# Kernel tuning notes

Hardware: AMD Instinct MI355X
Metric: run time of the kernel (lower is better)

Reference implementation:

```python
import jax, jax.numpy as jnp
import numpy as np

NUM_M = 2_000_000
NUM_T = 512
N = 16
NUM_GEN = N * (N - 1) // 2  # 120
NUM_STEPS = 64
TAU = 1.0


def _make_bases():
    # skew-symmetric so(n) basis, matching the torch buffer construction order
    bases = np.zeros((NUM_GEN, N, N), np.float32)
    k = 0
    for i in range(N):
        for j in range(i + 1, N):
            bases[k, i, j] = -1.0
            bases[k, j, i] = 1.0
            k += 1
    return jnp.asarray(bases)


def setup_inputs() -> dict:
    key = jax.random.key(0)
    ks = jax.random.split(key, 8)
    W = jax.random.normal(ks[0], (NUM_M, N), jnp.float32)
    emb_weight = W / jnp.linalg.norm(W, axis=-1, keepdims=True)  # normalized at init
    transition_coeffs = jax.random.normal(ks[1], (NUM_T, NUM_GEN), jnp.float32) * 0.1

    def lin(k, fi, fo):  # torch nn.Linear default init
        bound = 1.0 / np.sqrt(fi)
        kw, kb = jax.random.split(k)
        w = jax.random.uniform(kw, (fi, fo), jnp.float32, -bound, bound)
        b = jax.random.uniform(kb, (fo,), jnp.float32, -bound, bound)
        return w, b

    w1, b1 = lin(ks[2], 2 * N, 256)
    w2, b2 = lin(ks[3], 256, 128)
    w3, b3 = lin(ks[4], 128, NUM_T)

    v_src = jax.random.uniform(ks[5], (1, NUM_M), jnp.float32)
    v_target = jax.random.uniform(ks[6], (1, NUM_M), jnp.float32)
    # pre-sampled Gumbel(0,1) noise for gumbel_softmax, one draw per step
    u = jax.random.uniform(ks[7], (NUM_STEPS, 1, NUM_T), jnp.float32, 1e-6, 1.0 - 1e-6)
    gumbel = -jnp.log(-jnp.log(u))

    return {
        'v_src': v_src, 'v_target': v_target,
        'emb_weight': emb_weight, 'transition_coeffs': transition_coeffs,
        'bases': _make_bases(),
        'w1': w1, 'b1': b1, 'w2': w2, 'b2': b2, 'w3': w3, 'b3': b3,
        'gumbel': gumbel, 'num_steps': NUM_STEPS,
    }


def reference(v_src, v_target, emb_weight, transition_coeffs, bases,
              w1, b1, w2, b2, w3, b3, gumbel, num_steps):
    # training=True path of PetriNetAlignmentPredictor.forward, tau=1.0
    embs = emb_weight / jnp.linalg.norm(emb_weight, axis=-1, keepdims=True)
    v_cur = v_src @ embs      # [1, n]  (memory-bound matvec over num_m)
    v_tgt = v_target @ embs   # [1, n]
    gens = jnp.einsum('tg,gnm->tnm', transition_coeffs, bases)  # [num_t, n, n]
    expm_b = jax.vmap(jax.scipy.linalg.expm)

    def step(v, g):
        h = jax.nn.relu(jnp.concatenate([v, v_tgt], axis=-1) @ w1 + b1)
        h = jax.nn.relu(h @ w2 + b2)
        logits = h @ w3 + b3                       # [1, num_t]
        # gumbel_softmax(hard=True) with straight-through estimator
        y = jax.nn.softmax((logits + g) / TAU, axis=-1)
        hard = jax.nn.one_hot(jnp.argmax(y, axis=-1), logits.shape[-1], dtype=y.dtype)
        one_hot = hard + y - jax.lax.stop_gradient(y)
        omega = jnp.einsum('bt,tnm->bnm', one_hot, gens)  # skew-symmetric [1, n, n]
        R = expm_b(omega)
        v2 = jnp.einsum('bnm,bm->bn', R, v)
        v2 = v2 / jnp.linalg.norm(v2, axis=-1, keepdims=True)
        return v2, logits

    v_fin, logits_seq = jax.lax.scan(step, v_cur, gumbel[:num_steps])
    pred_marking = jax.nn.softmax(v_fin @ embs.T, axis=-1)  # [1, num_m]
    return pred_marking, logits_seq[:, 0, :]  # squeeze batch dim -> [num_steps, num_t]
```

## Files before the change

### kernel.cpp

```cpp
#include <hip/hip_runtime.h>

#define M_TOTAL   2000000
#define NT        512
#define K1_BLOCKS 2048

__device__ __forceinline__ float rlf(float v, int l) {
    union { float f; int i; } u; u.f = v;
    u.i = __builtin_amdgcn_readlane(u.i, l);
    return u.f;
}

#define REP16(M)  M(0) M(1) M(2) M(3) M(4) M(5) M(6) M(7) M(8) M(9) M(10) M(11) M(12) M(13) M(14) M(15)
#define REP16B(M) M(16) M(17) M(18) M(19) M(20) M(21) M(22) M(23) M(24) M(25) M(26) M(27) M(28) M(29) M(30) M(31)

#define VLD4(dst, base, c) { const volatile float* _p = (base) + 4*(c); \
    dst.x = _p[0]; dst.y = _p[1]; dst.z = _p[2]; dst.w = _p[3]; }

extern "C" __global__ __launch_bounds__(256)
void k_reduce(const float* __restrict__ emb, const float* __restrict__ vsrc,
              const float* __restrict__ vtgt, double* __restrict__ partials)
{
    const int tid = threadIdx.x;
    const int bid = blockIdx.x;
    double acc[32];
#pragma unroll
    for (int i = 0; i < 32; i++) acc[i] = 0.0;

    for (long long r = (long long)bid * 256 + tid; r < M_TOTAL; r += (long long)K1_BLOCKS * 256) {
        const float4* ep = (const float4*)(emb + r * 16);
        float4 e0 = ep[0], e1 = ep[1], e2 = ep[2], e3 = ep[3];
        float ev[16] = { e0.x,e0.y,e0.z,e0.w, e1.x,e1.y,e1.z,e1.w,
                         e2.x,e2.y,e2.z,e2.w, e3.x,e3.y,e3.z,e3.w };
        float n2 = 0.0f;
#pragma unroll
        for (int i = 0; i < 16; i++) n2 = fmaf(ev[i], ev[i], n2);
        float invn = 1.0f / sqrtf(n2);
        float s = vsrc[r];
        float t = vtgt[r];
#pragma unroll
        for (int i = 0; i < 16; i++) {
            float en = ev[i] * invn;
            acc[i]      += (double)s * (double)en;
            acc[16 + i] += (double)t * (double)en;
        }
    }
#pragma unroll
    for (int i = 0; i < 32; i++) {
        double v = acc[i];
#pragma unroll
        for (int off = 32; off; off >>= 1) v += __shfl_down(v, off);
        acc[i] = v;
    }
    __shared__ double lred[4][32];
    int lane = tid & 63, wv = tid >> 6;
    if (lane == 0) {
#pragma unroll
        for (int i = 0; i < 32; i++) lred[wv][i] = acc[i];
    }
    __syncthreads();
    if (tid < 32) {
        double v = lred[0][tid] + lred[1][tid] + lred[2][tid] + lred[3][tid];
        partials[(long long)bid * 32 + tid] = v;
    }
}

extern "C" __global__ __launch_bounds__(256)
void k_expm(const float* __restrict__ tc, float* __restrict__ Rtab)
{
    const int b = blockIdx.x;
    const int t = threadIdx.x;
    const int i = t >> 4, j = t & 15;
    __shared__ float Om[256];
    __shared__ float Ms[256];

    const float* crow = tc + b * 120;
    float o = 0.0f;
    if (i < j)      o = -crow[(i * (31 - i)) / 2 + (j - i - 1)];
    else if (i > j) o =  crow[(j * (31 - j)) / 2 + (i - j - 1)];
    Om[t] = o;
    Ms[t] = o;
    float s = (i == j ? 1.0f : 0.0f) + o;
    __syncthreads();

#pragma unroll
    for (int k = 2; k <= 16; k++) {
        float a0 = 0.0f, a1 = 0.0f, a2 = 0.0f, a3 = 0.0f;
#pragma unroll
        for (int m = 0; m < 4; m++) {
            a0 = fmaf(Om[i * 16 + m],      Ms[m * 16 + j],        a0);
            a1 = fmaf(Om[i * 16 + 4 + m],  Ms[(4 + m) * 16 + j],  a1);
            a2 = fmaf(Om[i * 16 + 8 + m],  Ms[(8 + m) * 16 + j],  a2);
            a3 = fmaf(Om[i * 16 + 12 + m], Ms[(12 + m) * 16 + j], a3);
        }
        float acc = ((a0 + a1) + (a2 + a3)) * (1.0f / (float)k);
        __syncthreads();
        Ms[t] = acc;
        s += acc;
        __syncthreads();
    }
    Rtab[b * 256 + t] = s;
}

extern "C" __global__ __launch_bounds__(128)
void k_prep(const float* __restrict__ w2g, const float* __restrict__ w3g,
            float* __restrict__ w2R, float* __restrict__ w3R)
{
    const int b = blockIdx.x, k = threadIdx.x;
    if (b < 512) {
        w3R[b * 128 + k] = w3g[k * 512 + b];
    } else {
        const int p2 = b - 512;
        const int j2 = k;
        for (int m = 0; m < 64; m++)
            w2R[(((p2 << 7) | j2) * 64) + m] = w2g[(64 * p2 + m) * 128 + j2];
    }
}

extern "C" __global__ __launch_bounds__(512, 2)
void k_steps(const double* __restrict__ partials,
             const float* __restrict__ w1g, const float* __restrict__ b1g,
             const float* __restrict__ b2g, const float* __restrict__ b3g,
             const float* __restrict__ w2R, const float* __restrict__ w3R,
             const float* __restrict__ Rtab, const float* __restrict__ gum,
             const int* __restrict__ nsp,
             float* __restrict__ outL, float* __restrict__ vf_out)
{
    __shared__ float w1s[32 * 256];
    __shared__ float b1s[256];
    __shared__ float b2s[128];
    __shared__ float h1s[256];
    __shared__ float h2s[128];
    __shared__ float h2p[512];
    __shared__ float xs[32];
    __shared__ float rkeys[8];
    __shared__ int   ridx[8];

    const int t = threadIdx.x;
    const int lane = t & 63;
    const int j2 = t & 127, p2 = t >> 7;

    const volatile float* w3v = (const volatile float*)(w3R + (size_t)t * 128);
    const volatile float* w2v = (const volatile float*)(w2R + (size_t)t * 64);
#define W3D(c) float4 w3_##c; VLD4(w3_##c, w3v, c)
    REP16(W3D) REP16B(W3D)
#undef W3D
#define W2D(c) float4 w2_##c; VLD4(w2_##c, w2v, c)
    REP16(W2D)
#undef W2D
    const float b3r = b3g[t];

    {
        int c = t >> 4, r = t & 15;
        double v = 0.0;
        for (int k = r; k < K1_BLOCKS; k += 16) v += partials[k * 32 + c];
        v += __shfl_xor(v, 1); v += __shfl_xor(v, 2);
        v += __shfl_xor(v, 4); v += __shfl_xor(v, 8);
        if (r == 0) xs[c] = (float)v;
    }
    for (int i = t; i < 8192; i += 512) w1s[i] = w1g[i];
    if (t < 256) b1s[t] = b1g[t];
    if (t < 128) b2s[t] = b2g[t];

    int ns = nsp[0];
    if (ns > 64) ns = 64;
    if (ns < 0)  ns = 0;

    float warm = 0.0f;
    for (int i = t; i < 512 * 256 / 4; i += 512) {
        float4 rv = ((const float4*)Rtab)[i];
        warm += (rv.x + rv.y) + (rv.z + rv.w);
    }
    if (ns == -2147483647) vf_out[0] = warm;

    __syncthreads();
    if (ns == 0 && t < 16) vf_out[t] = xs[t];

    const int i16 = t & 15, q4 = t >> 4;

    for (int step = 0; step < ns; step++) {
        float gv = gum[step * 512 + t];
        float xsreg = xs[t & 31];

        if (t < 256) {
            float a0 = b1s[t], a1 = 0.0f, a2 = 0.0f, a3 = 0.0f;
#pragma unroll
            for (int i = 0; i < 8; i++) {
                a0 = fmaf(rlf(xsreg, i),      w1s[i * 256 + t],        a0);
                a1 = fmaf(rlf(xsreg, 8 + i),  w1s[(8 + i) * 256 + t],  a1);
                a2 = fmaf(rlf(xsreg, 16 + i), w1s[(16 + i) * 256 + t], a2);
                a3 = fmaf(rlf(xsreg, 24 + i), w1s[(24 + i) * 256 + t], a3);
            }
            h1s[t] = fmaxf((a0 + a1) + (a2 + a3), 0.0f);
        }
        __syncthreads();

        {
            float h1seg = h1s[(p2 << 6) | lane];
            float a0 = 0.0f, a1 = 0.0f, a2 = 0.0f, a3 = 0.0f;
#define L2C(c) { a0 = fmaf(rlf(h1seg, 4*(c)+0), w2_##c.x, a0); \
                 a1 = fmaf(rlf(h1seg, 4*(c)+1), w2_##c.y, a1); \
                 a2 = fmaf(rlf(h1seg, 4*(c)+2), w2_##c.z, a2); \
                 a3 = fmaf(rlf(h1seg, 4*(c)+3), w2_##c.w, a3); }
            REP16(L2C)
#undef L2C
            h2p[(p2 << 7) | j2] = (a0 + a1) + (a2 + a3);
        }
        __syncthreads();
        if (t < 128) {
            float b = ((h2p[t] + h2p[128 + t]) + (h2p[256 + t] + h2p[384 + t])) + b2s[t];
            h2s[t] = fmaxf(b, 0.0f);
        }
        __syncthreads();

        float lg;
        {
            float h2lo = h2s[lane];
            float h2hi = h2s[64 + lane];
            float lg0 = 0.0f, lg1 = 0.0f, lg2 = 0.0f, lg3 = 0.0f;
#define L3LO(c) { lg0 = fmaf(rlf(h2lo, 4*(c)+0), w3_##c.x, lg0); \
                  lg1 = fmaf(rlf(h2lo, 4*(c)+1), w3_##c.y, lg1); \
                  lg2 = fmaf(rlf(h2lo, 4*(c)+2), w3_##c.z, lg2); \
                  lg3 = fmaf(rlf(h2lo, 4*(c)+3), w3_##c.w, lg3); }
#define L3HI(c) { lg0 = fmaf(rlf(h2hi, 4*(c)-64), w3_##c.x, lg0); \
                  lg1 = fmaf(rlf(h2hi, 4*(c)-63), w3_##c.y, lg1); \
                  lg2 = fmaf(rlf(h2hi, 4*(c)-62), w3_##c.z, lg2); \
                  lg3 = fmaf(rlf(h2hi, 4*(c)-61), w3_##c.w, lg3); }
            REP16(L3LO) REP16B(L3HI)
#undef L3LO
#undef L3HI
            lg = ((lg0 + lg1) + (lg2 + lg3)) + b3r;
        }
        outL[step * 512 + t] = lg;

        float key = lg + gv;
        int   idx = t;
#pragma unroll
        for (int off = 32; off; off >>= 1) {
            float ok = __shfl_down(key, off);
            int   oi = __shfl_down(idx, off);
            if (ok > key || (ok == key && oi < idx)) { key = ok; idx = oi; }
        }
        if (lane == 0) { rkeys[t >> 6] = key; ridx[t >> 6] = idx; }
        __syncthreads();

        if (t < 64) {
            float bk = rkeys[0]; int bi = ridx[0];
#pragma unroll
            for (int w = 1; w < 8; w++) {
                float ok = rkeys[w]; int oi = ridx[w];
                if (ok > bk || (ok == bk && oi < bi)) { bk = ok; bi = oi; }
            }
            const float4 rr = *(const float4*)(Rtab + bi * 256 + i16 * 16 + 4 * q4);
            float vv = xs[i16];
            float w0  = __shfl(vv, 20 * q4 + 0);
            float w1v = __shfl(vv, 20 * q4 + 1);
            float w2v = __shfl(vv, 20 * q4 + 2);
            float w3v = __shfl(vv, 20 * q4 + 3);
            float pr = rr.x * w0;
            pr = fmaf(rr.y, w1v, pr);
            pr = fmaf(rr.z, w2v, pr);
            pr = fmaf(rr.w, w3v, pr);
            pr += __shfl_xor(pr, 16);
            pr += __shfl_xor(pr, 32);
            float n2 = pr * pr;
            n2 += __shfl_xor(n2, 1);
            n2 += __shfl_xor(n2, 2);
            n2 += __shfl_xor(n2, 4);
            n2 += __shfl_xor(n2, 8);
            float invn = 1.0f / sqrtf(n2);
            float vn = pr * invn;
            if (t < 16) {
                xs[t] = vn;
                if (step == ns - 1) vf_out[t] = vn;
            }
        }
        __syncthreads();
    }
}

extern "C" __global__ __launch_bounds__(256)
void k_scores(const float* __restrict__ emb, const float* __restrict__ vf16,
              float* __restrict__ outP, double* __restrict__ sums)
{
    __shared__ float vfs[16];
    const int tid = threadIdx.x;
    const int bid = blockIdx.x;
    if (tid < 16) vfs[tid] = vf16[tid];
    __syncthreads();
    float v[16];
#pragma unroll
    for (int i = 0; i < 16; i++) v[i] = vfs[i];

    double bsum = 0.0;
    for (long long r = (long long)bid * 256 + tid; r < M_TOTAL; r += (long long)K1_BLOCKS * 256) {
        const float4* ep = (const float4*)(emb + r * 16);
        float4 e0 = ep[0], e1 = ep[1], e2 = ep[2], e3 = ep[3];
        float ev[16] = { e0.x,e0.y,e0.z,e0.w, e1.x,e1.y,e1.z,e1.w,
                         e2.x,e2.y,e2.z,e2.w, e3.x,e3.y,e3.z,e3.w };
        float n2 = 0.0f;
#pragma unroll
        for (int i = 0; i < 16; i++) n2 = fmaf(ev[i], ev[i], n2);
        float invn = 1.0f / sqrtf(n2);
        float dot = 0.0f;
#pragma unroll
        for (int i = 0; i < 16; i++) dot = fmaf(ev[i], v[i], dot);
        float e = expf(dot * invn);
        outP[r] = e;
        bsum += (double)e;
    }
#pragma unroll
    for (int off = 32; off; off >>= 1) bsum += __shfl_down(bsum, off);
    __shared__ double lred[4];
    if ((tid & 63) == 0) lred[tid >> 6] = bsum;
    __syncthreads();
    if (tid == 0) sums[bid] = lred[0] + lred[1] + lred[2] + lred[3];
}

extern "C" __global__ __launch_bounds__(256)
void k_total(const double* __restrict__ sums, double* __restrict__ invp)
{
    const int tid = threadIdx.x;
    double v = 0.0;
    for (int k = tid; k < K1_BLOCKS; k += 256) v += sums[k];
#pragma unroll
    for (int off = 32; off; off >>= 1) v += __shfl_down(v, off);
    __shared__ double lred[4];
    if ((tid & 63) == 0) lred[tid >> 6] = v;
    __syncthreads();
    if (tid == 0) invp[0] = 1.0 / (lred[0] + lred[1] + lred[2] + lred[3]);
}

extern "C" __global__ __launch_bounds__(256)
void k_scale(float* __restrict__ outP, const double* __restrict__ invp)
{
    const float inv = (float)invp[0];
    long long r4 = (long long)blockIdx.x * 256 + threadIdx.x;
    if (r4 < M_TOTAL / 4) {
        float4* p = (float4*)outP;
        float4 v = p[r4];
        v.x *= inv; v.y *= inv; v.z *= inv; v.w *= inv;
        p[r4] = v;
    }
}

extern "C" void kernel_launch(void* const* d_in, const int* in_sizes, int n_in,
                              void* d_out, int out_size, void* d_ws, size_t ws_size,
                              hipStream_t stream)
{
    const float* vsrc = (const float*)d_in[0];
    const float* vtgt = (const float*)d_in[1];
    const float* emb  = (const float*)d_in[2];
    const float* tc   = (const float*)d_in[3];
    const float* w1 = (const float*)d_in[5];
    const float* b1 = (const float*)d_in[6];
    const float* w2 = (const float*)d_in[7];
    const float* b2 = (const float*)d_in[8];
    const float* w3 = (const float*)d_in[9];
    const float* b3 = (const float*)d_in[10];
    const float* gum = (const float*)d_in[11];
    const int* nsp   = (const int*)d_in[12];

    float* outP = (float*)d_out;
    float* outL = outP + M_TOTAL;

    double* wsd      = (double*)d_ws;
    double* partials = wsd;
    double* sums     = wsd + K1_BLOCKS * 32;
    double* invp     = sums + K1_BLOCKS;
    float*  vf       = (float*)(invp + 1);

    float* Rtab = outP;
    float* w3R  = outP + 131072;
    float* w2R  = outP + 196608;

    k_expm<<<NT, 256, 0, stream>>>(tc, Rtab);
    k_prep<<<516, 128, 0, stream>>>(w2, w3, w2R, w3R);
    k_reduce<<<K1_BLOCKS, 256, 0, stream>>>(emb, vsrc, vtgt, partials);
    k_steps<<<1, 512, 0, stream>>>(partials, w1, b1, b2, b3, w2R, w3R, Rtab, gum, nsp, outL, vf);
    k_scores<<<K1_BLOCKS, 256, 0, stream>>>(emb, vf, outP, sums);
    k_total<<<1, 256, 0, stream>>>(sums, invp);
    k_scale<<<(M_TOTAL / 4 + 255) / 256, 256, 0, stream>>>(outP, invp);
}
```

Baseline: 562.3 us.

## Widen sequential step kernel to 1024 threads splitting MLP reductions

The single-block sequential step kernel now runs 1024 threads instead of 512. Each thread holds half as many register-resident weights for layers 2 and 3, and partial sums are combined through extra shared-memory buffers. k_prep is rewritten to produce the new weight layouts. The aim is to shorten the per-step serial latency of the MLP chain, at the cost of an extra barrier per step and more reduction traffic.

```diff
diff --git a/kernel.cpp b/kernel.cpp
--- a/kernel.cpp
+++ b/kernel.cpp
@@ -10,8 +10,8 @@
     return u.f;
 }
 
+#define REP8(M)   M(0) M(1) M(2) M(3) M(4) M(5) M(6) M(7)
 #define REP16(M)  M(0) M(1) M(2) M(3) M(4) M(5) M(6) M(7) M(8) M(9) M(10) M(11) M(12) M(13) M(14) M(15)
-#define REP16B(M) M(16) M(17) M(18) M(19) M(20) M(21) M(22) M(23) M(24) M(25) M(26) M(27) M(28) M(29) M(30) M(31)
 
 #define VLD4(dst, base, c) { const volatile float* _p = (base) + 4*(c); \
     dst.x = _p[0]; dst.y = _p[1]; dst.z = _p[2]; dst.w = _p[3]; }
@@ -101,22 +101,17 @@
     Rtab[b * 256 + t] = s;
 }
 
-extern "C" __global__ __launch_bounds__(128)
+extern "C" __global__ __launch_bounds__(64)
 void k_prep(const float* __restrict__ w2g, const float* __restrict__ w3g,
             float* __restrict__ w2R, float* __restrict__ w3R)
 {
     const int b = blockIdx.x, k = threadIdx.x;
-    if (b < 512) {
-        w3R[b * 128 + k] = w3g[k * 512 + b];
-    } else {
-        const int p2 = b - 512;
-        const int j2 = k;
-        for (int m = 0; m < 64; m++)
-            w2R[(((p2 << 7) | j2) * 64) + m] = w2g[(64 * p2 + m) * 128 + j2];
-    }
-}
-
-extern "C" __global__ __launch_bounds__(512, 2)
+    w3R[b * 64 + k] = w3g[((b >> 9) * 64 + k) * 512 + (b & 511)];
+    if (k < 32)
+        w2R[b * 32 + k] = w2g[((b >> 7) * 32 + k) * 128 + (b & 127)];
+}
+
+extern "C" __global__ __launch_bounds__(1024, 4)
 void k_steps(const double* __restrict__ partials,
              const float* __restrict__ w1g, const float* __restrict__ b1g,
              const float* __restrict__ b2g, const float* __restrict__ b3g,
@@ -128,9 +123,11 @@
     __shared__ float w1s[32 * 256];
     __shared__ float b1s[256];
     __shared__ float b2s[128];
+    __shared__ float b3s[512];
     __shared__ float h1s[256];
     __shared__ float h2s[128];
-    __shared__ float h2p[512];
+    __shared__ float h2p[1024];
+    __shared__ float lgp[1024];
     __shared__ float xs[32];
     __shared__ float rkeys[8];
     __shared__ int   ridx[8];
@@ -138,18 +135,18 @@
     const int t = threadIdx.x;
     const int lane = t & 63;
     const int j2 = t & 127, p2 = t >> 7;
-
-    const volatile float* w3v = (const volatile float*)(w3R + (size_t)t * 128);
-    const volatile float* w2v = (const volatile float*)(w2R + (size_t)t * 64);
+    const int col = t & 511, hf = t >> 9;
+
+    const volatile float* w3v = (const volatile float*)(w3R + (size_t)t * 64);
+    const volatile float* w2v = (const volatile float*)(w2R + (size_t)t * 32);
 #define W3D(c) float4 w3_##c; VLD4(w3_##c, w3v, c)
-    REP16(W3D) REP16B(W3D)
+    REP16(W3D)
 #undef W3D
 #define W2D(c) float4 w2_##c; VLD4(w2_##c, w2v, c)
-    REP16(W2D)
+    REP8(W2D)
 #undef W2D
-    const float b3r = b3g[t];
-
-    {
+
+    if (t < 512) {
         int c = t >> 4, r = t & 15;
         double v = 0.0;
         for (int k = r; k < K1_BLOCKS; k += 16) v += partials[k * 32 + c];
@@ -157,16 +154,17 @@
         v += __shfl_xor(v, 4); v += __shfl_xor(v, 8);
         if (r == 0) xs[c] = (float)v;
     }
-    for (int i = t; i < 8192; i += 512) w1s[i] = w1g[i];
+    for (int i = t; i < 8192; i += 1024) w1s[i] = w1g[i];
     if (t < 256) b1s[t] = b1g[t];
     if (t < 128) b2s[t] = b2g[t];
+    if (t < 512) b3s[t] = b3g[t];
 
     int ns = nsp[0];
     if (ns > 64) ns = 64;
     if (ns < 0)  ns = 0;
 
     float warm = 0.0f;
-    for (int i = t; i < 512 * 256 / 4; i += 512) {
+    for (int i = t; i < 512 * 256 / 4; i += 1024) {
         float4 rv = ((const float4*)Rtab)[i];
         warm += (rv.x + rv.y) + (rv.z + rv.w);
     }
@@ -178,7 +176,7 @@
     const int i16 = t & 15, q4 = t >> 4;
 
     for (int step = 0; step < ns; step++) {
-        float gv = gum[step * 512 + t];
+        float gv = (t < 512) ? gum[step * 512 + t] : 0.0f;
         float xsreg = xs[t & 31];
 
         if (t < 256) {
@@ -195,52 +193,51 @@
         __syncthreads();
 
         {
-            float h1seg = h1s[(p2 << 6) | lane];
+            float h1seg = h1s[(p2 << 5) | (lane & 31)];
             float a0 = 0.0f, a1 = 0.0f, a2 = 0.0f, a3 = 0.0f;
 #define L2C(c) { a0 = fmaf(rlf(h1seg, 4*(c)+0), w2_##c.x, a0); \
                  a1 = fmaf(rlf(h1seg, 4*(c)+1), w2_##c.y, a1); \
                  a2 = fmaf(rlf(h1seg, 4*(c)+2), w2_##c.z, a2); \
                  a3 = fmaf(rlf(h1seg, 4*(c)+3), w2_##c.w, a3); }
-            REP16(L2C)
+            REP8(L2C)
 #undef L2C
             h2p[(p2 << 7) | j2] = (a0 + a1) + (a2 + a3);
         }
         __syncthreads();
         if (t < 128) {
-            float b = ((h2p[t] + h2p[128 + t]) + (h2p[256 + t] + h2p[384 + t])) + b2s[t];
+            float b = (((h2p[t] + h2p[128 + t]) + (h2p[256 + t] + h2p[384 + t])) +
+                       ((h2p[512 + t] + h2p[640 + t]) + (h2p[768 + t] + h2p[896 + t]))) + b2s[t];
             h2s[t] = fmaxf(b, 0.0f);
         }
         __syncthreads();
 
-        float lg;
         {
-            float h2lo = h2s[lane];
-            float h2hi = h2s[64 + lane];
+            float h2seg = h2s[(hf << 6) | lane];
             float lg0 = 0.0f, lg1 = 0.0f, lg2 = 0.0f, lg3 = 0.0f;
-#define L3LO(c) { lg0 = fmaf(rlf(h2lo, 4*(c)+0), w3_##c.x, lg0); \
-                  lg1 = fmaf(rlf(h2lo, 4*(c)+1), w3_##c.y, lg1); \
-                  lg2 = fmaf(rlf(h2lo, 4*(c)+2), w3_##c.z, lg2); \
-                  lg3 = fmaf(rlf(h2lo, 4*(c)+3), w3_##c.w, lg3); }
-#define L3HI(c) { lg0 = fmaf(rlf(h2hi, 4*(c)-64), w3_##c.x, lg0); \
-                  lg1 = fmaf(rlf(h2hi, 4*(c)-63), w3_##c.y, lg1); \
-                  lg2 = fmaf(rlf(h2hi, 4*(c)-62), w3_##c.z, lg2); \
-                  lg3 = fmaf(rlf(h2hi, 4*(c)-61), w3_##c.w, lg3); }
-            REP16(L3LO) REP16B(L3HI)
-#undef L3LO
-#undef L3HI
-            lg = ((lg0 + lg1) + (lg2 + lg3)) + b3r;
-        }
-        outL[step * 512 + t] = lg;
-
-        float key = lg + gv;
-        int   idx = t;
-#pragma unroll
-        for (int off = 32; off; off >>= 1) {
-            float ok = __shfl_down(key, off);
-            int   oi = __shfl_down(idx, off);
-            if (ok > key || (ok == key && oi < idx)) { key = ok; idx = oi; }
-        }
-        if (lane == 0) { rkeys[t >> 6] = key; ridx[t >> 6] = idx; }
+#define L3C(c) { lg0 = fmaf(rlf(h2seg, 4*(c)+0), w3_##c.x, lg0); \
+                 lg1 = fmaf(rlf(h2seg, 4*(c)+1), w3_##c.y, lg1); \
+                 lg2 = fmaf(rlf(h2seg, 4*(c)+2), w3_##c.z, lg2); \
+                 lg3 = fmaf(rlf(h2seg, 4*(c)+3), w3_##c.w, lg3); }
+            REP16(L3C)
+#undef L3C
+            lgp[(hf << 9) | col] = (lg0 + lg1) + (lg2 + lg3);
+        }
+        __syncthreads();
+
+        if (t < 512) {
+            float lg = (lgp[t] + lgp[512 + t]) + b3s[t];
+            outL[step * 512 + t] = lg;
+
+            float key = lg + gv;
+            int   idx = t;
+#pragma unroll
+            for (int off = 32; off; off >>= 1) {
+                float ok = __shfl_down(key, off);
+                int   oi = __shfl_down(idx, off);
+                if (ok > key || (ok == key && oi < idx)) { key = ok; idx = oi; }
+            }
+            if (lane == 0) { rkeys[t >> 6] = key; ridx[t >> 6] = idx; }
+        }
         __syncthreads();
 
         if (t < 64) {
@@ -374,9 +371,9 @@
     float* w2R  = outP + 196608;
 
     k_expm<<<NT, 256, 0, stream>>>(tc, Rtab);
-    k_prep<<<516, 128, 0, stream>>>(w2, w3, w2R, w3R);
+    k_prep<<<1024, 64, 0, stream>>>(w2, w3, w2R, w3R);
     k_reduce<<<K1_BLOCKS, 256, 0, stream>>>(emb, vsrc, vtgt, partials);
-    k_steps<<<1, 512, 0, stream>>>(partials, w1, b1, b2, b3, w2R, w3R, Rtab, gum, nsp, outL, vf);
+    k_steps<<<1, 1024, 0, stream>>>(partials, w1, b1, b2, b3, w2R, w3R, Rtab, gum, nsp, outL, vf);
     k_scores<<<K1_BLOCKS, 256, 0, stream>>>(emb, vf, outP, sums);
     k_total<<<1, 256, 0, stream>>>(sums, invp);
     k_scale<<<(M_TOTAL / 4 + 255) / 256, 256, 0, stream>>>(outP, invp);
```

New measurement: 688.3 us. 22.4% more time.

## Split each embedding row across four lanes for coalesced float4 loads

Applied to the files above, without the earlier changes.

In the reduce and scores kernels, each row of 16 floats is now spread over four adjacent lanes, each loading one float4. The row norm and dot product are combined with xor-shuffles across those lanes. Consecutive lanes therefore read consecutive 16-byte chunks instead of strided 64-byte rows, which makes global loads fully coalesced and cuts per-thread double accumulators from 32 to 8. The cost is extra shuffles per row, a quarter of lanes idle on the scores store, and more loop iterations; the step kernel's launch bound is also rewritten as an explicit waves-per-EU attribute.

```diff
diff --git a/kernel.cpp b/kernel.cpp
--- a/kernel.cpp
+++ b/kernel.cpp
@@ -22,40 +22,43 @@
 {
     const int tid = threadIdx.x;
     const int bid = blockIdx.x;
-    double acc[32];
-#pragma unroll
-    for (int i = 0; i < 32; i++) acc[i] = 0.0;
-
-    for (long long r = (long long)bid * 256 + tid; r < M_TOTAL; r += (long long)K1_BLOCKS * 256) {
-        const float4* ep = (const float4*)(emb + r * 16);
-        float4 e0 = ep[0], e1 = ep[1], e2 = ep[2], e3 = ep[3];
-        float ev[16] = { e0.x,e0.y,e0.z,e0.w, e1.x,e1.y,e1.z,e1.w,
-                         e2.x,e2.y,e2.z,e2.w, e3.x,e3.y,e3.z,e3.w };
-        float n2 = 0.0f;
-#pragma unroll
-        for (int i = 0; i < 16; i++) n2 = fmaf(ev[i], ev[i], n2);
-        float invn = 1.0f / sqrtf(n2);
-        float s = vsrc[r];
-        float t = vtgt[r];
-#pragma unroll
-        for (int i = 0; i < 16; i++) {
-            float en = ev[i] * invn;
-            acc[i]      += (double)s * (double)en;
-            acc[16 + i] += (double)t * (double)en;
-        }
-    }
-#pragma unroll
-    for (int i = 0; i < 32; i++) {
-        double v = acc[i];
-#pragma unroll
-        for (int off = 32; off; off >>= 1) v += __shfl_down(v, off);
-        acc[i] = v;
+    const int q = tid & 3;
+    double aS[4], aT[4];
+#pragma unroll
+    for (int i = 0; i < 4; i++) { aS[i] = 0.0; aT[i] = 0.0; }
+
+    const float4* emb4 = (const float4*)emb;
+    for (long long f = (long long)bid * 256 + tid; f < (long long)M_TOTAL * 4;
+         f += (long long)K1_BLOCKS * 256) {
+        float4 e = emb4[f];
+        long long r = f >> 2;
+        float sq = fmaf(e.x, e.x, fmaf(e.y, e.y, fmaf(e.z, e.z, e.w * e.w)));
+        sq += __shfl_xor(sq, 1);
+        sq += __shfl_xor(sq, 2);
+        float invn = 1.0f / sqrtf(sq);
+        float s = vsrc[r] * invn;
+        float t = vtgt[r] * invn;
+        aS[0] += (double)(s * e.x); aS[1] += (double)(s * e.y);
+        aS[2] += (double)(s * e.z); aS[3] += (double)(s * e.w);
+        aT[0] += (double)(t * e.x); aT[1] += (double)(t * e.y);
+        aT[2] += (double)(t * e.z); aT[3] += (double)(t * e.w);
+    }
+#pragma unroll
+    for (int i = 0; i < 4; i++) {
+#pragma unroll
+        for (int off = 32; off >= 4; off >>= 1) {
+            aS[i] += __shfl_down(aS[i], off);
+            aT[i] += __shfl_down(aT[i], off);
+        }
     }
     __shared__ double lred[4][32];
     int lane = tid & 63, wv = tid >> 6;
-    if (lane == 0) {
-#pragma unroll
-        for (int i = 0; i < 32; i++) lred[wv][i] = acc[i];
+    if (lane < 4) {
+#pragma unroll
+        for (int i = 0; i < 4; i++) {
+            lred[wv][lane * 4 + i]      = aS[i];
+            lred[wv][16 + lane * 4 + i] = aT[i];
+        }
     }
     __syncthreads();
     if (tid < 32) {
@@ -116,7 +119,8 @@
     }
 }
 
-extern "C" __global__ __launch_bounds__(512, 2)
+extern "C" __global__ __launch_bounds__(512)
+__attribute__((amdgpu_waves_per_eu(2, 2)))
 void k_steps(const double* __restrict__ partials,
              const float* __restrict__ w1g, const float* __restrict__ b1g,
              const float* __restrict__ b2g, const float* __restrict__ b3g,
@@ -285,31 +289,29 @@
     __shared__ float vfs[16];
     const int tid = threadIdx.x;
     const int bid = blockIdx.x;
+    const int q = tid & 3;
     if (tid < 16) vfs[tid] = vf16[tid];
     __syncthreads();
-    float v[16];
-#pragma unroll
-    for (int i = 0; i < 16; i++) v[i] = vfs[i];
-
+    float v0 = vfs[q * 4 + 0], v1 = vfs[q * 4 + 1], v2 = vfs[q * 4 + 2], v3 = vfs[q * 4 + 3];
+
+    const float4* emb4 = (const float4*)emb;
     double bsum = 0.0;
-    for (long long r = (long long)bid * 256 + tid; r < M_TOTAL; r += (long long)K1_BLOCKS * 256) {
-        const float4* ep = (const float4*)(emb + r * 16);
-        float4 e0 = ep[0], e1 = ep[1], e2 = ep[2], e3 = ep[3];
-        float ev[16] = { e0.x,e0.y,e0.z,e0.w, e1.x,e1.y,e1.z,e1.w,
-                         e2.x,e2.y,e2.z,e2.w, e3.x,e3.y,e3.z,e3.w };
-        float n2 = 0.0f;
-#pragma unroll
-        for (int i = 0; i < 16; i++) n2 = fmaf(ev[i], ev[i], n2);
-        float invn = 1.0f / sqrtf(n2);
-        float dot = 0.0f;
-#pragma unroll
-        for (int i = 0; i < 16; i++) dot = fmaf(ev[i], v[i], dot);
-        float e = expf(dot * invn);
-        outP[r] = e;
-        bsum += (double)e;
-    }
-#pragma unroll
-    for (int off = 32; off; off >>= 1) bsum += __shfl_down(bsum, off);
+    for (long long f = (long long)bid * 256 + tid; f < (long long)M_TOTAL * 4;
+         f += (long long)K1_BLOCKS * 256) {
+        float4 e = emb4[f];
+        long long r = f >> 2;
+        float sq = fmaf(e.x, e.x, fmaf(e.y, e.y, fmaf(e.z, e.z, e.w * e.w)));
+        float d  = fmaf(e.x, v0, fmaf(e.y, v1, fmaf(e.z, v2, e.w * v3)));
+        sq += __shfl_xor(sq, 1);  d += __shfl_xor(d, 1);
+        sq += __shfl_xor(sq, 2);  d += __shfl_xor(d, 2);
+        float ex = expf(d / sqrtf(sq));
+        if (q == 0) {
+            outP[r] = ex;
+            bsum += (double)ex;
+        }
+    }
+#pragma unroll
+    for (int off = 4; off <= 32; off <<= 1) bsum += __shfl_down(bsum, off);
     __shared__ double lred[4];
     if ((tid & 63) == 0) lred[tid >> 6] = bsum;
     __syncthreads();
```

After: 558.3 us. About the same (-0.7%).
